# Optimization experiments

Measured on AMD Instinct MI355X. Metric: run time of the kernel, lower is better.

The kernel has to match this reference:

```python
import jax, jax.numpy as jnp
import numpy as np

N = 200000   # nodes
E = 6400000  # edges (avg degree 32)
F_IN = 128
N_CLASSES = 4
DIMS = [F_IN, 24, 12, 6, 4, 2]


def setup_inputs() -> dict:
    key = jax.random.key(0)
    ks = jax.random.split(key, 16)
    inp = {}
    inp['x'] = jax.random.normal(ks[0], (N, F_IN), dtype=jnp.float32)
    inp['edge_index'] = jax.random.randint(ks[1], (2, E), 0, N, dtype=jnp.int32)
    for i in range(5):
        fan_in = DIMS[i]
        inp[f'W{i+1}'] = jax.random.normal(ks[2 + i], (DIMS[i], DIMS[i + 1]), dtype=jnp.float32) / np.float32(np.sqrt(fan_in))
        inp[f'b{i+1}'] = jnp.zeros((DIMS[i + 1],), dtype=jnp.float32)
    inp['Wc'] = jax.random.normal(ks[8], (2, N_CLASSES), dtype=jnp.float32) / np.float32(np.sqrt(2.0))
    inp['bc'] = jnp.zeros((N_CLASSES,), dtype=jnp.float32)
    return inp


def _gcn_forward(x, row, col, norm, weights, biases, Wc, bc):
    h = x
    for W, b in zip(weights, biases):
        xl = h @ W                               # [N, d_out] linear transform first (d_out <= d_in)
        msg = norm[:, None] * xl[row]            # gather + normalize: [E+N, d_out]
        agg = jax.ops.segment_max(msg, col, num_segments=N)  # aggr='max'
        h = jnp.tanh(agg + b)
    out = h @ Wc + bc
    return out, h


def reference(x, edge_index, W1, b1, W2, b2, W3, b3, W4, b4, W5, b5, Wc, bc):
    loops = jnp.arange(N, dtype=edge_index.dtype)
    row = jnp.concatenate([edge_index[0], loops])  # source (with self loops)
    col = jnp.concatenate([edge_index[1], loops])  # target
    # symmetric GCN normalization on A + I
    deg = jax.ops.segment_sum(jnp.ones_like(col, dtype=jnp.float32), col, num_segments=N)
    dinv = jnp.where(deg > 0, jax.lax.rsqrt(deg), 0.0)
    norm = dinv[row] * dinv[col]                   # [E+N]
    weights = [W1, W2, W3, W4, W5]
    biases = [b1, b2, b3, b4, b5]
    return _gcn_forward(x, row, col, norm, weights, biases, Wc, bc)
```

## Files before the change

### kernel.cpp

```cpp
#include <hip/hip_runtime.h>
#include <cmath>

#define NN 200000
#define EE 6400000
#define NBKT 391
#define GRID_A 512
#define BLK_A 256


__global__ __launch_bounds__(BLK_A) void count_buckets_kernel(const int* __restrict__ col,
                                                              int* __restrict__ blkhist) {
    __shared__ int h[NBKT];
    for (int t = threadIdx.x; t < NBKT; t += BLK_A) h[t] = 0;
    __syncthreads();
    const int4* col4 = (const int4*)col;
    for (int i = blockIdx.x * BLK_A + threadIdx.x; i < EE / 4; i += GRID_A * BLK_A) {
        int4 c = col4[i];
        atomicAdd(&h[c.x >> 9], 1);
        atomicAdd(&h[c.y >> 9], 1);
        atomicAdd(&h[c.z >> 9], 1);
        atomicAdd(&h[c.w >> 9], 1);
    }
    __syncthreads();
    for (int t = threadIdx.x; t < NBKT; t += BLK_A) blkhist[blockIdx.x * NBKT + t] = h[t];
}

__global__ __launch_bounds__(GRID_A) void scan_cols_kernel(int* __restrict__ blkhist,
                                                           int* __restrict__ btot) {
    __shared__ int sc[GRID_A];
    int bkt = blockIdx.x, t = threadIdx.x;
    int v = blkhist[t * NBKT + bkt];
    sc[t] = v;
    __syncthreads();
    for (int off = 1; off < GRID_A; off <<= 1) {
        int add = (t >= off) ? sc[t - off] : 0;
        __syncthreads();
        sc[t] += add;
        __syncthreads();
    }
    blkhist[t * NBKT + bkt] = sc[t] - v;
    if (t == GRID_A - 1) btot[bkt] = sc[t];
}

__global__ __launch_bounds__(512) void scan_btot_kernel(const int* __restrict__ btot,
                                                        int* __restrict__ bbase) {
    __shared__ int sc[512];
    int t = threadIdx.x;
    int v = (t < NBKT) ? btot[t] : 0;
    sc[t] = v;
    __syncthreads();
    for (int off = 1; off < 512; off <<= 1) {
        int add = (t >= off) ? sc[t - off] : 0;
        __syncthreads();
        sc[t] += add;
        __syncthreads();
    }
    if (t < NBKT) bbase[t] = sc[t] - v;
    if (t == NBKT - 1) bbase[NBKT] = sc[t];
}

__global__ __launch_bounds__(BLK_A) void place_pairs_kernel(const int* __restrict__ row,
                                                            const int* __restrict__ col,
                                                            const int* __restrict__ blkhist,
                                                            const int* __restrict__ bbase,
                                                            unsigned int* __restrict__ pairs) {
    __shared__ int cur[NBKT];
    for (int t = threadIdx.x; t < NBKT; t += BLK_A)
        cur[t] = bbase[t] + blkhist[blockIdx.x * NBKT + t];
    __syncthreads();
    const int4* col4 = (const int4*)col;
    const int4* row4 = (const int4*)row;
    for (int i = blockIdx.x * BLK_A + threadIdx.x; i < EE / 4; i += GRID_A * BLK_A) {
        int4 c = col4[i];
        int4 r = row4[i];
        int p0 = atomicAdd(&cur[c.x >> 9], 1);
        pairs[p0] = (unsigned int)r.x | ((unsigned int)(c.x & 511) << 18);
        int p1 = atomicAdd(&cur[c.y >> 9], 1);
        pairs[p1] = (unsigned int)r.y | ((unsigned int)(c.y & 511) << 18);
        int p2 = atomicAdd(&cur[c.z >> 9], 1);
        pairs[p2] = (unsigned int)r.z | ((unsigned int)(c.z & 511) << 18);
        int p3 = atomicAdd(&cur[c.w >> 9], 1);
        pairs[p3] = (unsigned int)r.w | ((unsigned int)(c.w & 511) << 18);
    }
}

__global__ __launch_bounds__(512) void bucket_build_kernel(const unsigned int* __restrict__ pairs,
                                                           const int* __restrict__ bbase,
                                                           int* __restrict__ deg,
                                                           int* __restrict__ offs,
                                                           float* __restrict__ dinv,
                                                           int* __restrict__ row_sorted) {
    __shared__ int h[512];
    __shared__ int sc[512];
    int b = blockIdx.x, tid = threadIdx.x;
    int base = bbase[b], end = bbase[b + 1];
    int node0 = b << 9;
    int nloc = NN - node0; if (nloc > 512) nloc = 512;

    h[tid] = 0;
    __syncthreads();
    for (int i = base + tid; i < end; i += 512) atomicAdd(&h[pairs[i] >> 18], 1);
    __syncthreads();

    int v = h[tid];
    sc[tid] = v;
    __syncthreads();
    for (int off = 1; off < 512; off <<= 1) {
        int add = (tid >= off) ? sc[tid - off] : 0;
        __syncthreads();
        sc[tid] += add;
        __syncthreads();
    }
    int excl = sc[tid] - v;

    if (tid < nloc) {
        deg[node0 + tid]  = v;
        offs[node0 + tid] = base + excl;
        dinv[node0 + tid] = rsqrtf((float)(v + 1));
    }
    __syncthreads();
    h[tid] = base + excl;
    __syncthreads();
    for (int i = base + tid; i < end; i += 512) {
        unsigned int p = pairs[i];
        int pos = atomicAdd(&h[p >> 18], 1);
        row_sorted[pos] = (int)(p & 0x3FFFFu);
    }
}

__global__ void matmul128_y_kernel(const float* __restrict__ x, const float* __restrict__ W,
                                   const float* __restrict__ dinv, float* __restrict__ y, int n) {
    __shared__ float Ws[128 * 24];
    for (int t = threadIdx.x; t < 128 * 24; t += blockDim.x) Ws[t] = W[t];
    __syncthreads();
    int i = blockIdx.x * blockDim.x + threadIdx.x;
    if (i >= n) return;
    float acc[24];
#pragma unroll
    for (int j = 0; j < 24; ++j) acc[j] = 0.f;
    const float4* hr = (const float4*)(x + (size_t)i * 128);
#pragma unroll 8
    for (int k4 = 0; k4 < 32; ++k4) {
        float4 hv = hr[k4];
        const float* wk = &Ws[k4 * 4 * 24];
#pragma unroll
        for (int j = 0; j < 24; ++j) acc[j] += hv.x * wk[j];
#pragma unroll
        for (int j = 0; j < 24; ++j) acc[j] += hv.y * wk[24 + j];
#pragma unroll
        for (int j = 0; j < 24; ++j) acc[j] += hv.z * wk[48 + j];
#pragma unroll
        for (int j = 0; j < 24; ++j) acc[j] += hv.w * wk[72 + j];
    }
    float di = dinv[i];
    float4* orow = (float4*)(y + (size_t)i * 24);
#pragma unroll
    for (int q = 0; q < 6; ++q) {
        float4 o;
        o.x = di * acc[q * 4 + 0];
        o.y = di * acc[q * 4 + 1];
        o.z = di * acc[q * 4 + 2];
        o.w = di * acc[q * 4 + 3];
        orow[q] = o;
    }
}

template<int DOUT, int DNEXT, int VEC>
__global__ __launch_bounds__(256) void gather_fused_kernel(const int* __restrict__ offs,
                                                           const int* __restrict__ deg,
                                                           const int* __restrict__ row_sorted,
                                                           const float* __restrict__ dinv,
                                                           const float* __restrict__ y,
                                                           const float* __restrict__ b,
                                                           const float* __restrict__ Wn,
                                                           float* __restrict__ ynext) {
    constexpr int LPN = DOUT / VEC;
    constexpr int NPB = 256 / LPN;
    typedef float vec_t __attribute__((ext_vector_type(VEC)));

    __shared__ float hs[NPB * DOUT];
    __shared__ float dcs[NPB];

    int ln = threadIdx.x / LPN;
    int j  = threadIdx.x % LPN;
    int node = blockIdx.x * NPB + ln;
    bool active = (ln < NPB) && (node < NN);

    if (active) {
        float dc = dinv[node];
        const vec_t* yv = (const vec_t*)y;
        vec_t m = yv[(size_t)node * LPN + j];
        int s = offs[node];
        int e = s + deg[node];
        int k = s;
        for (; k + 7 < e; k += 8) {
            int r[8];
#pragma unroll
            for (int u = 0; u < 8; ++u) r[u] = row_sorted[k + u];
            vec_t v[8];
#pragma unroll
            for (int u = 0; u < 8; ++u) v[u] = yv[(size_t)r[u] * LPN + j];
#pragma unroll
            for (int c = 0; c < VEC; ++c) {
                float a0 = fmaxf(fmaxf(v[0][c], v[1][c]), fmaxf(v[2][c], v[3][c]));
                float a1 = fmaxf(fmaxf(v[4][c], v[5][c]), fmaxf(v[6][c], v[7][c]));
                m[c] = fmaxf(m[c], fmaxf(a0, a1));
            }
        }
        for (; k + 3 < e; k += 4) {
            int r0 = row_sorted[k];
            int r1 = row_sorted[k + 1];
            int r2 = row_sorted[k + 2];
            int r3 = row_sorted[k + 3];
            vec_t v0 = yv[(size_t)r0 * LPN + j];
            vec_t v1 = yv[(size_t)r1 * LPN + j];
            vec_t v2 = yv[(size_t)r2 * LPN + j];
            vec_t v3 = yv[(size_t)r3 * LPN + j];
#pragma unroll
            for (int c = 0; c < VEC; ++c)
                m[c] = fmaxf(m[c], fmaxf(fmaxf(v0[c], v1[c]), fmaxf(v2[c], v3[c])));
        }
        for (; k < e; ++k) {
            vec_t v0 = yv[(size_t)row_sorted[k] * LPN + j];
#pragma unroll
            for (int c = 0; c < VEC; ++c) m[c] = fmaxf(m[c], v0[c]);
        }
#pragma unroll
        for (int c = 0; c < VEC; ++c)
            hs[ln * DOUT + j * VEC + c] = tanhf(dc * m[c] + b[j * VEC + c]);
        if (j == 0) dcs[ln] = dc;
    }
    __syncthreads();

    for (int idx = threadIdx.x; idx < NPB * DNEXT; idx += 256) {
        int ln2 = idx / DNEXT;
        int j2 = idx - ln2 * DNEXT;
        int gn = blockIdx.x * NPB + ln2;
        if (gn < NN) {
            float acc = 0.f;
#pragma unroll
            for (int k = 0; k < DOUT; ++k) acc += hs[ln2 * DOUT + k] * Wn[k * DNEXT + j2];
            ynext[(size_t)gn * DNEXT + j2] = dcs[ln2] * acc;
        }
    }
}

__global__ __launch_bounds__(256) void gather_fused4_kernel(const int* __restrict__ offs,
                                                            const int* __restrict__ deg,
                                                            const int* __restrict__ row_sorted,
                                                            const float* __restrict__ dinv,
                                                            const float* __restrict__ y,
                                                            const float* __restrict__ b,
                                                            const float* __restrict__ Wn,
                                                            float* __restrict__ ynext) {
    int node = blockIdx.x * 256 + threadIdx.x;
    if (node >= NN) return;
    float dc = dinv[node];
    const float4* yv = (const float4*)y;
    float4 m = yv[node];
    int s = offs[node];
    int e = s + deg[node];
    int k = s;
    for (; k + 7 < e; k += 8) {
        int r[8];
#pragma unroll
        for (int u = 0; u < 8; ++u) r[u] = row_sorted[k + u];
        float4 v[8];
#pragma unroll
        for (int u = 0; u < 8; ++u) v[u] = yv[r[u]];
        float ax, ay, az, aw, bx, by, bz, bw;
        ax = fmaxf(fmaxf(v[0].x, v[1].x), fmaxf(v[2].x, v[3].x));
        bx = fmaxf(fmaxf(v[4].x, v[5].x), fmaxf(v[6].x, v[7].x));
        ay = fmaxf(fmaxf(v[0].y, v[1].y), fmaxf(v[2].y, v[3].y));
        by = fmaxf(fmaxf(v[4].y, v[5].y), fmaxf(v[6].y, v[7].y));
        az = fmaxf(fmaxf(v[0].z, v[1].z), fmaxf(v[2].z, v[3].z));
        bz = fmaxf(fmaxf(v[4].z, v[5].z), fmaxf(v[6].z, v[7].z));
        aw = fmaxf(fmaxf(v[0].w, v[1].w), fmaxf(v[2].w, v[3].w));
        bw = fmaxf(fmaxf(v[4].w, v[5].w), fmaxf(v[6].w, v[7].w));
        m.x = fmaxf(m.x, fmaxf(ax, bx));
        m.y = fmaxf(m.y, fmaxf(ay, by));
        m.z = fmaxf(m.z, fmaxf(az, bz));
        m.w = fmaxf(m.w, fmaxf(aw, bw));
    }
    for (; k + 3 < e; k += 4) {
        float4 v0 = yv[row_sorted[k]];
        float4 v1 = yv[row_sorted[k + 1]];
        float4 v2 = yv[row_sorted[k + 2]];
        float4 v3 = yv[row_sorted[k + 3]];
        m.x = fmaxf(m.x, fmaxf(fmaxf(v0.x, v1.x), fmaxf(v2.x, v3.x)));
        m.y = fmaxf(m.y, fmaxf(fmaxf(v0.y, v1.y), fmaxf(v2.y, v3.y)));
        m.z = fmaxf(m.z, fmaxf(fmaxf(v0.z, v1.z), fmaxf(v2.z, v3.z)));
        m.w = fmaxf(m.w, fmaxf(fmaxf(v0.w, v1.w), fmaxf(v2.w, v3.w)));
    }
    for (; k < e; ++k) {
        float4 v0 = yv[row_sorted[k]];
        m.x = fmaxf(m.x, v0.x); m.y = fmaxf(m.y, v0.y);
        m.z = fmaxf(m.z, v0.z); m.w = fmaxf(m.w, v0.w);
    }
    float h0 = tanhf(dc * m.x + b[0]);
    float h1 = tanhf(dc * m.y + b[1]);
    float h2 = tanhf(dc * m.z + b[2]);
    float h3 = tanhf(dc * m.w + b[3]);
    float2 o;
    o.x = dc * (h0 * Wn[0] + h1 * Wn[2] + h2 * Wn[4] + h3 * Wn[6]);
    o.y = dc * (h0 * Wn[1] + h1 * Wn[3] + h2 * Wn[5] + h3 * Wn[7]);
    ((float2*)ynext)[node] = o;
}

__global__ __launch_bounds__(256) void gather_final_kernel(const int* __restrict__ offs,
                                                           const int* __restrict__ deg,
                                                           const int* __restrict__ row_sorted,
                                                           const float* __restrict__ dinv,
                                                           const float* __restrict__ y,
                                                           const float* __restrict__ b,
                                                           const float* __restrict__ Wc,
                                                           const float* __restrict__ bc,
                                                           float* __restrict__ out,
                                                           float* __restrict__ hout) {
    int node = blockIdx.x * 256 + threadIdx.x;
    if (node >= NN) return;
    float dc = dinv[node];
    const float2* yv = (const float2*)y;
    float2 m = yv[node];
    int s = offs[node];
    int e = s + deg[node];
    int k = s;
    for (; k + 7 < e; k += 8) {
        int r[8];
#pragma unroll
        for (int u = 0; u < 8; ++u) r[u] = row_sorted[k + u];
        float2 v[8];
#pragma unroll
        for (int u = 0; u < 8; ++u) v[u] = yv[r[u]];
        float ax = fmaxf(fmaxf(v[0].x, v[1].x), fmaxf(v[2].x, v[3].x));
        float bx = fmaxf(fmaxf(v[4].x, v[5].x), fmaxf(v[6].x, v[7].x));
        float ay = fmaxf(fmaxf(v[0].y, v[1].y), fmaxf(v[2].y, v[3].y));
        float by = fmaxf(fmaxf(v[4].y, v[5].y), fmaxf(v[6].y, v[7].y));
        m.x = fmaxf(m.x, fmaxf(ax, bx));
        m.y = fmaxf(m.y, fmaxf(ay, by));
    }
    for (; k + 3 < e; k += 4) {
        float2 v0 = yv[row_sorted[k]];
        float2 v1 = yv[row_sorted[k + 1]];
        float2 v2 = yv[row_sorted[k + 2]];
        float2 v3 = yv[row_sorted[k + 3]];
        m.x = fmaxf(m.x, fmaxf(fmaxf(v0.x, v1.x), fmaxf(v2.x, v3.x)));
        m.y = fmaxf(m.y, fmaxf(fmaxf(v0.y, v1.y), fmaxf(v2.y, v3.y)));
    }
    for (; k < e; ++k) {
        float2 v0 = yv[row_sorted[k]];
        m.x = fmaxf(m.x, v0.x); m.y = fmaxf(m.y, v0.y);
    }
    float h0 = tanhf(dc * m.x + b[0]);
    float h1 = tanhf(dc * m.y + b[1]);
    float2 ho; ho.x = h0; ho.y = h1;
    ((float2*)hout)[node] = ho;
    float4 o;
    o.x = h0 * Wc[0] + h1 * Wc[4] + bc[0];
    o.y = h0 * Wc[1] + h1 * Wc[5] + bc[1];
    o.z = h0 * Wc[2] + h1 * Wc[6] + bc[2];
    o.w = h0 * Wc[3] + h1 * Wc[7] + bc[3];
    ((float4*)out)[node] = o;
}

extern "C" void kernel_launch(void* const* d_in, const int* in_sizes, int n_in,
                              void* d_out, int out_size, void* d_ws, size_t ws_size,
                              hipStream_t stream) {
    const float* x  = (const float*)d_in[0];
    const int*   ei = (const int*)d_in[1];
    const int* row = ei;
    const int* col = ei + EE;
    const float* W1 = (const float*)d_in[2];  const float* b1 = (const float*)d_in[3];
    const float* W2 = (const float*)d_in[4];  const float* b2 = (const float*)d_in[5];
    const float* W3 = (const float*)d_in[6];  const float* b3 = (const float*)d_in[7];
    const float* W4 = (const float*)d_in[8];  const float* b4 = (const float*)d_in[9];
    const float* W5 = (const float*)d_in[10]; const float* b5 = (const float*)d_in[11];
    const float* Wc = (const float*)d_in[12]; const float* bc = (const float*)d_in[13];
    float* out = (float*)d_out;

    char* ws = (char*)d_ws;
    int*          deg        = (int*)(ws + 0);
    float*        dinv       = (float*)(ws + 800000);
    int*          offs       = (int*)(ws + 1600000);
    int*          bbase      = (int*)(ws + 2400000);
    int*          blkhist    = (int*)(ws + 2402048);
    int*          btot       = (int*)(ws + 3204864);
    unsigned int* pairs      = (unsigned int*)(ws + 3206912);
    float*        bufB       = (float*)(ws + 3206912);
    int*          row_sorted = (int*)(ws + 28806912);
    float*        bufA       = (float*)(ws + 54406912);

    const int BLK = 256;
    const int gN = (NN + BLK - 1) / BLK;

    count_buckets_kernel<<<GRID_A, BLK_A, 0, stream>>>(col, blkhist);
    scan_cols_kernel<<<NBKT, GRID_A, 0, stream>>>(blkhist, btot);
    scan_btot_kernel<<<1, 512, 0, stream>>>(btot, bbase);
    place_pairs_kernel<<<GRID_A, BLK_A, 0, stream>>>(row, col, blkhist, bbase, pairs);
    bucket_build_kernel<<<NBKT, 512, 0, stream>>>(pairs, bbase, deg, offs, dinv, row_sorted);

    matmul128_y_kernel<<<gN, BLK, 0, stream>>>(x, W1, dinv, bufB, NN);

    {
        constexpr int NPB = 256 / (24 / 4);
        gather_fused_kernel<24, 12, 4><<<(NN + NPB - 1) / NPB, 256, 0, stream>>>(
            offs, deg, row_sorted, dinv, bufB, b1, W2, bufA);
    }
    {
        constexpr int NPB = 256 / (12 / 4);
        gather_fused_kernel<12, 6, 4><<<(NN + NPB - 1) / NPB, 256, 0, stream>>>(
            offs, deg, row_sorted, dinv, bufA, b2, W3, bufB);
    }
    {
        constexpr int NPB = 256 / (6 / 2);
        gather_fused_kernel<6, 4, 2><<<(NN + NPB - 1) / NPB, 256, 0, stream>>>(
            offs, deg, row_sorted, dinv, bufB, b3, W4, bufA);
    }
    gather_fused4_kernel<<<gN, BLK, 0, stream>>>(offs, deg, row_sorted, dinv, bufA, b4, W5, bufB);

    gather_final_kernel<<<gN, BLK, 0, stream>>>(offs, deg, row_sorted, dinv, bufB, b5, Wc, bc,
                                                out, out + (size_t)NN * 4);
}
```

Measured before the change: 795.0 us.

## Sort neighbor lists by source range and gather in block-synchronized row bands

The CSR build now sub-buckets each destination's edges by source-row band (25 bands of 8192 rows), so every neighbor list is ordered by source band. The gather kernel walks the bands in lockstep, with a block barrier after each band, so all threads in a block touch the same slice of y at once and that slice stays in cache. In exchange the CSR build needs a much larger shared histogram (512×25 ints), the gather loses its 8-wide unrolled loads, and it adds 25 barriers per block, which cuts memory-level parallelism and adds divergence.

```diff
diff --git a/kernel.cpp b/kernel.cpp
--- a/kernel.cpp
+++ b/kernel.cpp
@@ -6,6 +6,8 @@
 #define NBKT 391
 #define GRID_A 512
 #define BLK_A 256
+#define RB_SHIFT 13
+#define NRB 25
 
 
 __global__ __launch_bounds__(BLK_A) void count_buckets_kernel(const int* __restrict__ col,
@@ -90,20 +92,28 @@
                                                            int* __restrict__ offs,
                                                            float* __restrict__ dinv,
                                                            int* __restrict__ row_sorted) {
-    __shared__ int h[512];
+    __shared__ int h2[512 * NRB];
     __shared__ int sc[512];
     int b = blockIdx.x, tid = threadIdx.x;
     int base = bbase[b], end = bbase[b + 1];
     int node0 = b << 9;
     int nloc = NN - node0; if (nloc > 512) nloc = 512;
 
-    h[tid] = 0;
-    __syncthreads();
-    for (int i = base + tid; i < end; i += 512) atomicAdd(&h[pairs[i] >> 18], 1);
-    __syncthreads();
-
-    int v = h[tid];
-    sc[tid] = v;
+    for (int t = tid; t < 512 * NRB; t += 512) h2[t] = 0;
+    __syncthreads();
+    for (int i = base + tid; i < end; i += 512) {
+        unsigned int p = pairs[i];
+        atomicAdd(&h2[(p >> 18) * NRB + ((p & 0x3FFFFu) >> RB_SHIFT)], 1);
+    }
+    __syncthreads();
+
+    int acc = 0;
+    for (int r = 0; r < NRB; ++r) {
+        int c = h2[tid * NRB + r];
+        h2[tid * NRB + r] = acc;
+        acc += c;
+    }
+    sc[tid] = acc;
     __syncthreads();
     for (int off = 1; off < 512; off <<= 1) {
         int add = (tid >= off) ? sc[tid - off] : 0;
@@ -111,20 +121,21 @@
         sc[tid] += add;
         __syncthreads();
     }
-    int excl = sc[tid] - v;
+    int excl = sc[tid] - acc;
 
     if (tid < nloc) {
-        deg[node0 + tid]  = v;
+        deg[node0 + tid]  = acc;
         offs[node0 + tid] = base + excl;
-        dinv[node0 + tid] = rsqrtf((float)(v + 1));
-    }
-    __syncthreads();
-    h[tid] = base + excl;
-    __syncthreads();
+        dinv[node0 + tid] = rsqrtf((float)(acc + 1));
+    }
+    for (int r = 0; r < NRB; ++r) h2[tid * NRB + r] += base + excl;
+    __syncthreads();
+
     for (int i = base + tid; i < end; i += 512) {
         unsigned int p = pairs[i];
-        int pos = atomicAdd(&h[p >> 18], 1);
-        row_sorted[pos] = (int)(p & 0x3FFFFu);
+        int rw = (int)(p & 0x3FFFFu);
+        int pos = atomicAdd(&h2[(p >> 18) * NRB + (rw >> RB_SHIFT)], 1);
+        row_sorted[pos] = rw;
     }
 }
 
@@ -186,45 +197,36 @@
     int node = blockIdx.x * NPB + ln;
     bool active = (ln < NPB) && (node < NN);
 
+    const vec_t* yv = (const vec_t*)y;
+    vec_t m;
+#pragma unroll
+    for (int c = 0; c < VEC; ++c) m[c] = 0.f;
+    float dc = 0.f;
+    int k = 0, e = 0;
+    int curRow = 0x7FFFFFFF;
+
     if (active) {
-        float dc = dinv[node];
-        const vec_t* yv = (const vec_t*)y;
-        vec_t m = yv[(size_t)node * LPN + j];
-        int s = offs[node];
-        int e = s + deg[node];
-        int k = s;
-        for (; k + 7 < e; k += 8) {
-            int r[8];
-#pragma unroll
-            for (int u = 0; u < 8; ++u) r[u] = row_sorted[k + u];
-            vec_t v[8];
-#pragma unroll
-            for (int u = 0; u < 8; ++u) v[u] = yv[(size_t)r[u] * LPN + j];
-#pragma unroll
-            for (int c = 0; c < VEC; ++c) {
-                float a0 = fmaxf(fmaxf(v[0][c], v[1][c]), fmaxf(v[2][c], v[3][c]));
-                float a1 = fmaxf(fmaxf(v[4][c], v[5][c]), fmaxf(v[6][c], v[7][c]));
-                m[c] = fmaxf(m[c], fmaxf(a0, a1));
-            }
+        dc = dinv[node];
+        m = yv[(size_t)node * LPN + j];
+        k = offs[node];
+        e = k + deg[node];
+        if (k < e) curRow = row_sorted[k];
+    }
+
+    for (int rb = 0; rb < NRB; ++rb) {
+        int bend = (rb + 1) << RB_SHIFT;
+        while (curRow < bend) {
+            vec_t v = yv[(size_t)curRow * LPN + j];
+            ++k;
+            int nr = (k < e) ? row_sorted[k] : 0x7FFFFFFF;
+#pragma unroll
+            for (int c = 0; c < VEC; ++c) m[c] = fmaxf(m[c], v[c]);
+            curRow = nr;
         }
-        for (; k + 3 < e; k += 4) {
-            int r0 = row_sorted[k];
-            int r1 = row_sorted[k + 1];
-            int r2 = row_sorted[k + 2];
-            int r3 = row_sorted[k + 3];
-            vec_t v0 = yv[(size_t)r0 * LPN + j];
-            vec_t v1 = yv[(size_t)r1 * LPN + j];
-            vec_t v2 = yv[(size_t)r2 * LPN + j];
-            vec_t v3 = yv[(size_t)r3 * LPN + j];
-#pragma unroll
-            for (int c = 0; c < VEC; ++c)
-                m[c] = fmaxf(m[c], fmaxf(fmaxf(v0[c], v1[c]), fmaxf(v2[c], v3[c])));
-        }
-        for (; k < e; ++k) {
-            vec_t v0 = yv[(size_t)row_sorted[k] * LPN + j];
-#pragma unroll
-            for (int c = 0; c < VEC; ++c) m[c] = fmaxf(m[c], v0[c]);
-        }
+        __syncthreads();
+    }
+
+    if (active) {
 #pragma unroll
         for (int c = 0; c < VEC; ++c)
             hs[ln * DOUT + j * VEC + c] = tanhf(dc * m[c] + b[j * VEC + c]);
@@ -239,7 +241,7 @@
         if (gn < NN) {
             float acc = 0.f;
 #pragma unroll
-            for (int k = 0; k < DOUT; ++k) acc += hs[ln2 * DOUT + k] * Wn[k * DNEXT + j2];
+            for (int k2 = 0; k2 < DOUT; ++k2) acc += hs[ln2 * DOUT + k2] * Wn[k2 * DNEXT + j2];
             ynext[(size_t)gn * DNEXT + j2] = dcs[ln2] * acc;
         }
     }
```

New measurement: 848.8 us. 6.8% more time.
